# Kernel optimization log

Hardware: AMD Instinct MI355X
Metric: run time of the kernel (lower is better)

Reference implementation:

```python
import jax, jax.numpy as jnp
import numpy as np

C = 512
CQK = C // 8
B, H, W = 4, 128, 128

def setup_inputs() -> dict:
    key = jax.random.key(0)
    ks = jax.random.split(key, 8)
    x = jax.random.normal(ks[0], (B, C, H, W), dtype=jnp.float32)
    # 1x1 conv weights stored as [out, in]
    Wq = jax.random.normal(ks[1], (CQK, C), dtype=jnp.float32) * (1.0 / np.sqrt(C))
    bq = jax.random.normal(ks[2], (CQK,), dtype=jnp.float32) * 0.01
    Wk = jax.random.normal(ks[3], (CQK, C), dtype=jnp.float32) * (1.0 / np.sqrt(C))
    bk = jax.random.normal(ks[4], (CQK,), dtype=jnp.float32) * 0.01
    Wv = jax.random.normal(ks[5], (C, C), dtype=jnp.float32) * (1.0 / np.sqrt(C))
    bv = jax.random.normal(ks[6], (C,), dtype=jnp.float32) * 0.01
    gamma = jnp.zeros((1,), dtype=jnp.float32)
    return {"x": x, "Wq": Wq, "bq": bq, "Wk": Wk, "bk": bk, "Wv": Wv, "bv": bv, "gamma": gamma}

def _conv1x1(x, Wt, b):
    # x: [B,C,H,W], Wt: [O,C] -> [B,O,H,W]
    return jnp.einsum('bchw,oc->bohw', x, Wt) + b[None, :, None, None]

def reference(x, Wq, bq, Wk, bk, Wv, bv, gamma):
    q = _conv1x1(x, Wq, bq)   # [B,CQK,H,W]
    k = _conv1x1(x, Wk, bk)   # [B,CQK,H,W]
    v = _conv1x1(x, Wv, bv)   # [B,C,H,W]
    # axial attention along height, independently per (batch, width-column)
    energy = jnp.einsum('bchw,bcgw->bwhg', q, k)      # [B,W,H,H]
    attn = jax.nn.softmax(energy, axis=-1)
    out = jnp.einsum('bcgw,bwhg->bchw', v, attn)      # [B,C,H,W]
    return gamma * out + x
```

## Files before the change

### kernel.cpp

```cpp
#include <hip/hip_runtime.h>
#include <hip/hip_bf16.h>

typedef float f32x4  __attribute__((ext_vector_type(4)));
typedef int   v8i    __attribute__((ext_vector_type(8)));
typedef unsigned short u16;
typedef unsigned char  u8;

#define B_ 4
#define C_ 512
#define H_ 128
#define W_ 128
#define NO_ 640

__device__ __forceinline__ u16 f2bf(float f) {
    __hip_bfloat16 h = __float2bfloat16(f);
    union { __hip_bfloat16 h; u16 u; } cv; cv.h = h; return cv.u;
}
__device__ __forceinline__ unsigned f2fp8x2(float a, float b) {
    return (unsigned)__builtin_amdgcn_cvt_pk_fp8_f32(a, b, 0, false);
}
__device__ __forceinline__ u8 f2fp8(float f) {
    return (u8)(f2fp8x2(f, 0.f) & 0xFF);
}
__device__ __forceinline__ float fp82f(unsigned b) {
    const unsigned s = (b >> 7) & 1u, e = (b >> 3) & 15u, m = b & 7u;
    union { unsigned u; float f; } c;
    c.u = (s << 31) | ((e + 120u) << 23) | (m << 20);
    const float fs = (s ? -1.f : 1.f) * (float)m * 0.001953125f;
    return e ? c.f : fs;
}

__device__ __forceinline__ void gld16(const void* g, void* l) {
    __builtin_amdgcn_global_load_lds(
        (const __attribute__((address_space(1))) void*)g,
        (__attribute__((address_space(3))) void*)l, 16, 0, 0);
}

__global__ __launch_bounds__(256) void k_convw(const float* __restrict__ Wq, const float* __restrict__ bq,
                                               const float* __restrict__ Wk, const float* __restrict__ bk,
                                               const float* __restrict__ Wv, const float* __restrict__ bv,
                                               u8* __restrict__ Wcat, float* __restrict__ bcat) {
    const int idx = blockIdx.x * 256 + threadIdx.x;
    if (idx < NO_ * C_) {
        const int o = idx >> 9, c = idx & 511;
        float v;
        if (o < 64)       v = Wq[o * C_ + c];
        else if (o < 128) v = Wk[(o - 64) * C_ + c];
        else              v = Wv[(o - 128) * C_ + c];
        Wcat[idx] = f2fp8(v);
    }
    if (idx < NO_) {
        float v = (idx < 64) ? bq[idx] : ((idx < 128) ? bk[idx - 64] : bv[idx - 128]);
        bcat[idx] = v;
    }
}

__global__ __launch_bounds__(256) void k_transpose_x(const float* __restrict__ x, u8* __restrict__ xT) {
    __shared__ float tile[64][65];
    const int b  = blockIdx.x >> 7;
    const int h  = blockIdx.x & 127;
    const int c0 = (blockIdx.y >> 1) * 64;
    const int w0 = (blockIdx.y & 1) * 64;
    const int t = threadIdx.x, r = t >> 4, seg = t & 15;
    const float* xp = x + (size_t)b * C_ * H_ * W_ + (size_t)h * W_;
#pragma unroll
    for (int rr = 0; rr < 4; ++rr) {
        const int c = rr * 16 + r;
        float4 v = *(const float4*)(xp + (size_t)(c0 + c) * (H_ * W_) + w0 + seg * 4);
        tile[c][seg * 4 + 0] = v.x; tile[c][seg * 4 + 1] = v.y;
        tile[c][seg * 4 + 2] = v.z; tile[c][seg * 4 + 3] = v.w;
    }
    __syncthreads();
#pragma unroll
    for (int rr = 0; rr < 4; ++rr) {
        const int w = rr * 16 + r;
        const unsigned lo = f2fp8x2(tile[seg * 4 + 0][w], tile[seg * 4 + 1][w]);
        const unsigned hi = f2fp8x2(tile[seg * 4 + 2][w], tile[seg * 4 + 3][w]);
        *(unsigned*)(xT + ((size_t)((b * W_ + w0 + w) * H_ + h)) * C_ + c0 + seg * 4)
            = (lo & 0xFFFFu) | (hi << 16);
    }
}

__global__ __launch_bounds__(256, 2) void k_gemm(const u8* __restrict__ A, const u8* __restrict__ Wc,
                                                 const float* __restrict__ bias, u8* __restrict__ Call,
                                                 u8* __restrict__ vt) {
    __shared__ __align__(16) u8 smem[65536];
    const int t = threadIdx.x;
    const int lane = t & 63;
    const int wave = t >> 6;
    const int wr = wave >> 1;
    const int wc = wave & 1;
    const int lr = lane & 15;
    const int q4 = lane >> 4;

    const int bid = blockIdx.x;
    const int wg = (bid & 7) * 320 + (bid >> 3);
    const int panel = wg / 5;
    const int n = wg - panel * 5;
    const int r0 = panel * 128;
    const int n0 = n * 128;

    const int srow = t >> 3;
    const int slog = (t & 7) ^ (srow & 7);
    const u8* gA = A  + (size_t)(r0 + srow) * C_ + slog * 16;
    const u8* gB = Wc + (size_t)(n0 + srow) * C_ + slog * 16;

#define STAGE(KT) do {                                                   \
        u8* S_ = smem + ((KT) & 1) * 32768;                              \
        const int k0_ = (KT) * 128;                                      \
        gld16(gA + k0_,                    S_ + t * 16);                 \
        gld16(gA + (size_t)32 * C_ + k0_,  S_ + 4096  + t * 16);         \
        gld16(gA + (size_t)64 * C_ + k0_,  S_ + 8192  + t * 16);         \
        gld16(gA + (size_t)96 * C_ + k0_,  S_ + 12288 + t * 16);         \
        gld16(gB + k0_,                    S_ + 16384 + t * 16);         \
        gld16(gB + (size_t)32 * C_ + k0_,  S_ + 20480 + t * 16);         \
        gld16(gB + (size_t)64 * C_ + k0_,  S_ + 24576 + t * 16);         \
        gld16(gB + (size_t)96 * C_ + k0_,  S_ + 28672 + t * 16);         \
    } while (0)

    f32x4 acc[4][4] = {};
    STAGE(0);

#pragma unroll
    for (int T = 0; T < 4; ++T) {
        asm volatile("s_waitcnt vmcnt(0)" ::: "memory");
        __builtin_amdgcn_s_barrier();
        const u8* Ab = smem + (T & 1) * 32768;
        const u8* Bb = Ab + 16384;
        v8i fa[4], fb[4];
#pragma unroll
        for (int mi = 0; mi < 4; ++mi) {
            const int rr = wr * 64 + mi * 16 + lr;
            int4 lo = *(const int4*)&Ab[rr * 128 + (((2 * q4 + 0) ^ (rr & 7)) * 16)];
            int4 hi = *(const int4*)&Ab[rr * 128 + (((2 * q4 + 1) ^ (rr & 7)) * 16)];
            v8i f; f[0] = lo.x; f[1] = lo.y; f[2] = lo.z; f[3] = lo.w;
                   f[4] = hi.x; f[5] = hi.y; f[6] = hi.z; f[7] = hi.w;
            fa[mi] = f;
        }
#pragma unroll
        for (int ni = 0; ni < 4; ++ni) {
            const int rr = wc * 64 + ni * 16 + lr;
            int4 lo = *(const int4*)&Bb[rr * 128 + (((2 * q4 + 0) ^ (rr & 7)) * 16)];
            int4 hi = *(const int4*)&Bb[rr * 128 + (((2 * q4 + 1) ^ (rr & 7)) * 16)];
            v8i f; f[0] = lo.x; f[1] = lo.y; f[2] = lo.z; f[3] = lo.w;
                   f[4] = hi.x; f[5] = hi.y; f[6] = hi.z; f[7] = hi.w;
            fb[ni] = f;
        }
        if (T < 3) STAGE(T + 1);
        __builtin_amdgcn_s_setprio(1);
#pragma unroll
        for (int mi = 0; mi < 4; ++mi)
#pragma unroll
            for (int ni = 0; ni < 4; ++ni)
                acc[mi][ni] = __builtin_amdgcn_mfma_scale_f32_16x16x128_f8f6f4(
                    fa[mi], fb[ni], acc[mi][ni],
                    0, 0,
                    0, 0x7F7F7F7Fu,
                    0, 0x7F7F7F7Fu);
        __builtin_amdgcn_s_setprio(0);
    }
#undef STAGE
    __syncthreads();

    if (n == 0) {
#pragma unroll
        for (int ni = 0; ni < 4; ++ni) {
            const int o = wc * 64 + ni * 16 + lr;
            const float bz = bias[o];
#pragma unroll
            for (int mi = 0; mi < 4; ++mi)
#pragma unroll
                for (int j = 0; j < 4; ++j) {
                    const int rg = r0 + wr * 64 + mi * 16 + q4 * 4 + j;
                    Call[(size_t)rg * 128 + o] = f2fp8(acc[mi][ni][j] + bz);
                }
        }
    } else {
        u8* Tt = smem;
#pragma unroll
        for (int ni = 0; ni < 4; ++ni) {
            const int c_loc = wc * 64 + ni * 16 + lr;
            const float bz = bias[n0 + c_loc];
#pragma unroll
            for (int mi = 0; mi < 4; ++mi) {
                const int h = wr * 64 + mi * 16 + q4 * 4;
                unsigned p = f2fp8x2(acc[mi][ni][0] + bz, acc[mi][ni][1] + bz) & 0xFFFFu;
                p |= f2fp8x2(acc[mi][ni][2] + bz, acc[mi][ni][3] + bz) << 16;
                *(unsigned*)&Tt[c_loc * 144 + h] = p;
            }
        }
        __syncthreads();
        {
            const int c_loc = t >> 1;
            const int half  = t & 1;
            const int cg = (n - 1) * 128 + c_loc;
            u8* dst = vt + ((size_t)panel * 512 + cg) * 128 + half * 64;
            const u8* src = &Tt[c_loc * 144 + half * 64];
#pragma unroll
            for (int k = 0; k < 4; ++k)
                *(int4*)&dst[k * 16] = *(const int4*)&src[k * 16];
        }
    }
}

__global__ __launch_bounds__(256) void k_attn(const u8* __restrict__ Call, const u8* __restrict__ vt,
                                              u8* __restrict__ outws) {
    __shared__ __align__(16) float E[128][132];
    __shared__ float Rinv[128];
    const int bw = blockIdx.x;
    const int t = threadIdx.x;
    const int lane = t & 63;
    const int wr = t >> 7;
    const int wc = (t >> 6) & 1;
    const int lr = lane & 15, lk = (lane >> 4) * 8;
    const size_t rowbase = (size_t)bw * 128;

    f32x4 e[4][4] = {};
#pragma unroll
    for (int kk = 0; kk < 2; ++kk) {
        long fq[4], fk[4];
#pragma unroll
        for (int mi = 0; mi < 4; ++mi)
            fq[mi] = *(const long*)&Call[(rowbase + wr * 64 + mi * 16 + lr) * 128 + kk * 32 + lk];
#pragma unroll
        for (int ni = 0; ni < 4; ++ni)
            fk[ni] = *(const long*)&Call[(rowbase + wc * 64 + ni * 16 + lr) * 128 + 64 + kk * 32 + lk];
#pragma unroll
        for (int mi = 0; mi < 4; ++mi)
#pragma unroll
            for (int ni = 0; ni < 4; ++ni)
                e[mi][ni] = __builtin_amdgcn_mfma_f32_16x16x32_fp8_fp8(fq[mi], fk[ni], e[mi][ni], 0, 0, 0);
    }
#pragma unroll
    for (int mi = 0; mi < 4; ++mi)
#pragma unroll
        for (int ni = 0; ni < 4; ++ni)
#pragma unroll
            for (int j = 0; j < 4; ++j)
                E[wr * 64 + mi * 16 + (lane >> 4) * 4 + j][wc * 64 + ni * 16 + lr] = e[mi][ni][j];
    __syncthreads();

    {
        const int h = t >> 1, hf = (t & 1) * 64;
        float m = -1e30f;
        for (int i = 0; i < 64; ++i) m = fmaxf(m, E[h][hf + i]);
        m = fmaxf(m, __shfl_xor(m, 1));
        float s = 0.f;
        for (int i = 0; i < 64; ++i) {
            float p = __expf(E[h][hf + i] - m);
            E[h][hf + i] = p;
            s += p;
        }
        s += __shfl_xor(s, 1);
        if ((t & 1) == 0) Rinv[h] = 1.0f / s;
    }
    __syncthreads();

    float rv[4][4];
#pragma unroll
    for (int mi = 0; mi < 4; ++mi)
#pragma unroll
        for (int j = 0; j < 4; ++j)
            rv[mi][j] = Rinv[wr * 64 + mi * 16 + (lane >> 4) * 4 + j];

    long pa[4][4];
#pragma unroll
    for (int kk = 0; kk < 4; ++kk)
#pragma unroll
        for (int mi = 0; mi < 4; ++mi) {
            const float* ep = &E[wr * 64 + mi * 16 + lr][kk * 32 + lk];
            float4 v0 = *(const float4*)ep;
            float4 v1 = *(const float4*)(ep + 4);
            unsigned lo = (unsigned)__builtin_amdgcn_cvt_pk_fp8_f32(v0.x, v0.y, 0, false);
            lo = (unsigned)__builtin_amdgcn_cvt_pk_fp8_f32(v0.z, v0.w, (int)lo, true);
            unsigned hi = (unsigned)__builtin_amdgcn_cvt_pk_fp8_f32(v1.x, v1.y, 0, false);
            hi = (unsigned)__builtin_amdgcn_cvt_pk_fp8_f32(v1.z, v1.w, (int)hi, true);
            pa[kk][mi] = (long)lo | ((long)hi << 32);
        }

    for (int cc = 0; cc < 4; ++cc) {
        f32x4 acc[4][4] = {};
#pragma unroll
        for (int kk = 0; kk < 4; ++kk) {
            long fb[4];
#pragma unroll
            for (int ni = 0; ni < 4; ++ni)
                fb[ni] = *(const long*)&vt[((size_t)bw * 512 + cc * 128 + wc * 64 + ni * 16 + lr) * 128 + kk * 32 + lk];
#pragma unroll
            for (int mi = 0; mi < 4; ++mi)
#pragma unroll
                for (int ni = 0; ni < 4; ++ni)
                    acc[mi][ni] = __builtin_amdgcn_mfma_f32_16x16x32_fp8_fp8(pa[kk][mi], fb[ni], acc[mi][ni], 0, 0, 0);
        }
#pragma unroll
        for (int ni = 0; ni < 4; ++ni) {
            const int c = cc * 128 + wc * 64 + ni * 16 + lr;
#pragma unroll
            for (int mi = 0; mi < 4; ++mi)
#pragma unroll
                for (int j = 0; j < 4; ++j) {
                    const int hh = wr * 64 + mi * 16 + (lane >> 4) * 4 + j;
                    outws[(rowbase + hh) * 512 + c] = f2fp8(acc[mi][ni][j] * rv[mi][j]);
                }
        }
    }
}

__global__ __launch_bounds__(256) void k_merge(const u8* __restrict__ outws, const float* __restrict__ x,
                                               const float* __restrict__ gamma, float* __restrict__ out) {
    __shared__ float tile[64][65];
    const int b  = blockIdx.x >> 7;
    const int h  = blockIdx.x & 127;
    const int c0 = (blockIdx.y >> 1) * 64;
    const int w0 = (blockIdx.y & 1) * 64;
    const float g = gamma[0];
    const int t = threadIdx.x, r = t >> 4, seg = t & 15;
#pragma unroll
    for (int rr = 0; rr < 4; ++rr) {
        const int w = rr * 16 + r;
        unsigned v = *(const unsigned*)(outws + ((size_t)((b * W_ + w0 + w) * H_) + h) * C_ + c0 + seg * 4);
        tile[w][seg * 4 + 0] = fp82f(v & 0xFFu);
        tile[w][seg * 4 + 1] = fp82f((v >> 8) & 0xFFu);
        tile[w][seg * 4 + 2] = fp82f((v >> 16) & 0xFFu);
        tile[w][seg * 4 + 3] = fp82f(v >> 24);
    }
    __syncthreads();
#pragma unroll
    for (int rr = 0; rr < 4; ++rr) {
        const int c = rr * 16 + r;
        const size_t base = ((size_t)(b * C_ + c0 + c) * H_ + h) * W_ + w0 + seg * 4;
        float4 xv = *(const float4*)(x + base);
        float4 o;
        o.x = g * tile[seg * 4 + 0][c] + xv.x;
        o.y = g * tile[seg * 4 + 1][c] + xv.y;
        o.z = g * tile[seg * 4 + 2][c] + xv.z;
        o.w = g * tile[seg * 4 + 3][c] + xv.w;
        *(float4*)(out + base) = o;
    }
}

extern "C" void kernel_launch(void* const* d_in, const int* in_sizes, int n_in,
                              void* d_out, int out_size, void* d_ws, size_t ws_size,
                              hipStream_t stream) {
    const float* x     = (const float*)d_in[0];
    const float* Wq    = (const float*)d_in[1];
    const float* bq    = (const float*)d_in[2];
    const float* Wk    = (const float*)d_in[3];
    const float* bk    = (const float*)d_in[4];
    const float* Wv    = (const float*)d_in[5];
    const float* bv    = (const float*)d_in[6];
    const float* gamma = (const float*)d_in[7];

    char* ws = (char*)d_ws;
    u8*    Wcat  = (u8*)ws;
    float* bcat  = (float*)(ws + 655360);
    u8*    xT    = (u8*)(ws + (1u << 20));
    u8*    Call  = (u8*)(ws + (1u << 20) + 67108864);
    u8*    outws = (u8*)(ws + (1u << 20));
    u8*    vt    = (u8*)d_out;

    k_convw<<<dim3((NO_ * C_ + 255) / 256), 256, 0, stream>>>(Wq, bq, Wk, bk, Wv, bv, Wcat, bcat);
    k_transpose_x<<<dim3(B_ * H_, 16), 256, 0, stream>>>(x, xT);
    k_gemm<<<dim3(2560), 256, 0, stream>>>(xT, Wcat, bcat, Call, vt);
    k_attn<<<dim3(B_ * W_), 256, 0, stream>>>(Call, vt, outws);
    k_merge<<<dim3(B_ * H_, 16), 256, 0, stream>>>(outws, x, gamma, (float*)d_out);
}
```

Baseline: 154.5 us.

## Keep A panel resident in LDS and loop over all output column tiles per block

The GEMM now assigns one block per 128-row panel, loading the full 128x512 fp8 A panel into LDS once and streaming the five 128-column weight tiles through a double-buffered ring. Previously five separate blocks re-read the same A panel from global memory. The trade-off is fewer blocks (512 instead of 2560), about 114 KB of LDS per block so only one block fits per CU, and a longer serial chain of work per block with an extra barrier for each epilogue.

```diff
diff --git a/kernel.cpp b/kernel.cpp
--- a/kernel.cpp
+++ b/kernel.cpp
@@ -81,10 +81,13 @@
     }
 }
 
-__global__ __launch_bounds__(256, 2) void k_gemm(const u8* __restrict__ A, const u8* __restrict__ Wc,
-                                                 const float* __restrict__ bias, u8* __restrict__ Call,
-                                                 u8* __restrict__ vt) {
-    __shared__ __align__(16) u8 smem[65536];
+__global__ __launch_bounds__(256) void k_gemm(const u8* __restrict__ A, const u8* __restrict__ Wc,
+                                              const float* __restrict__ bias, u8* __restrict__ Call,
+                                              u8* __restrict__ vt) {
+    __shared__ __align__(16) u8 smem[116736];
+    u8* Asm   = smem;
+    u8* Bring = smem + 65536;
+    u8* Tt    = smem + 98304;
     const int t = threadIdx.x;
     const int lane = t & 63;
     const int wave = t >> 6;
@@ -93,50 +96,54 @@
     const int lr = lane & 15;
     const int q4 = lane >> 4;
 
-    const int bid = blockIdx.x;
-    const int wg = (bid & 7) * 320 + (bid >> 3);
-    const int panel = wg / 5;
-    const int n = wg - panel * 5;
+    const int panel = blockIdx.x;
     const int r0 = panel * 128;
-    const int n0 = n * 128;
-
-    const int srow = t >> 3;
-    const int slog = (t & 7) ^ (srow & 7);
-    const u8* gA = A  + (size_t)(r0 + srow) * C_ + slog * 16;
-    const u8* gB = Wc + (size_t)(n0 + srow) * C_ + slog * 16;
-
-#define STAGE(KT) do {                                                   \
-        u8* S_ = smem + ((KT) & 1) * 32768;                              \
-        const int k0_ = (KT) * 128;                                      \
-        gld16(gA + k0_,                    S_ + t * 16);                 \
-        gld16(gA + (size_t)32 * C_ + k0_,  S_ + 4096  + t * 16);         \
-        gld16(gA + (size_t)64 * C_ + k0_,  S_ + 8192  + t * 16);         \
-        gld16(gA + (size_t)96 * C_ + k0_,  S_ + 12288 + t * 16);         \
-        gld16(gB + k0_,                    S_ + 16384 + t * 16);         \
-        gld16(gB + (size_t)32 * C_ + k0_,  S_ + 20480 + t * 16);         \
-        gld16(gB + (size_t)64 * C_ + k0_,  S_ + 24576 + t * 16);         \
-        gld16(gB + (size_t)96 * C_ + k0_,  S_ + 28672 + t * 16);         \
+
+    const u8* gA = A + (size_t)(r0 + (t >> 5)) * C_ + (((t & 31) ^ ((t >> 5) & 7)) * 16);
+    const int brow = t >> 3;
+    const u8* gBbase = Wc + (size_t)brow * C_ + (((t & 7) ^ (brow & 7)) * 16);
+
+#define STAGE_B(NN, TT, SLOT) do {                                       \
+        u8* S_ = Bring + (SLOT) * 16384;                                 \
+        const u8* src_ = gBbase + (size_t)(NN) * 128 * C_ + (TT) * 128;  \
+        gld16(src_,          S_ + t * 16);                               \
+        gld16(src_ + 16384,  S_ + 4096  + t * 16);                       \
+        gld16(src_ + 32768,  S_ + 8192  + t * 16);                       \
+        gld16(src_ + 49152,  S_ + 12288 + t * 16);                       \
     } while (0)
 
-    f32x4 acc[4][4] = {};
-    STAGE(0);
-
-#pragma unroll
-    for (int T = 0; T < 4; ++T) {
+#pragma unroll
+    for (int r = 0; r < 16; ++r)
+        gld16(gA + (size_t)r * 4096, Asm + r * 4096 + t * 16);
+    STAGE_B(0, 0, 0);
+
+    f32x4 acc[4][4];
+
+#pragma unroll
+    for (int s = 0; s < 20; ++s) {
+        const int nn = s >> 2, TT = s & 3, slot = s & 1;
+        if (TT == 0) {
+#pragma unroll
+            for (int mi = 0; mi < 4; ++mi)
+#pragma unroll
+                for (int ni = 0; ni < 4; ++ni)
+                    acc[mi][ni] = (f32x4){0.f, 0.f, 0.f, 0.f};
+        }
         asm volatile("s_waitcnt vmcnt(0)" ::: "memory");
         __builtin_amdgcn_s_barrier();
-        const u8* Ab = smem + (T & 1) * 32768;
-        const u8* Bb = Ab + 16384;
+
         v8i fa[4], fb[4];
 #pragma unroll
         for (int mi = 0; mi < 4; ++mi) {
             const int rr = wr * 64 + mi * 16 + lr;
-            int4 lo = *(const int4*)&Ab[rr * 128 + (((2 * q4 + 0) ^ (rr & 7)) * 16)];
-            int4 hi = *(const int4*)&Ab[rr * 128 + (((2 * q4 + 1) ^ (rr & 7)) * 16)];
+            const int base = rr * 512 + TT * 128;
+            int4 lo = *(const int4*)&Asm[base + (((2 * q4 + 0) ^ (rr & 7)) * 16)];
+            int4 hi = *(const int4*)&Asm[base + (((2 * q4 + 1) ^ (rr & 7)) * 16)];
             v8i f; f[0] = lo.x; f[1] = lo.y; f[2] = lo.z; f[3] = lo.w;
                    f[4] = hi.x; f[5] = hi.y; f[6] = hi.z; f[7] = hi.w;
             fa[mi] = f;
         }
+        const u8* Bb = Bring + slot * 16384;
 #pragma unroll
         for (int ni = 0; ni < 4; ++ni) {
             const int rr = wc * 64 + ni * 16 + lr;
@@ -146,7 +153,8 @@
                    f[4] = hi.x; f[5] = hi.y; f[6] = hi.z; f[7] = hi.w;
             fb[ni] = f;
         }
-        if (T < 3) STAGE(T + 1);
+        if (s + 1 < 20) STAGE_B((s + 1) >> 2, (s + 1) & 3, (s + 1) & 1);
+
         __builtin_amdgcn_s_setprio(1);
 #pragma unroll
         for (int mi = 0; mi < 4; ++mi)
@@ -158,49 +166,51 @@
                     0, 0x7F7F7F7Fu,
                     0, 0x7F7F7F7Fu);
         __builtin_amdgcn_s_setprio(0);
-    }
-#undef STAGE
-    __syncthreads();
-
-    if (n == 0) {
-#pragma unroll
-        for (int ni = 0; ni < 4; ++ni) {
-            const int o = wc * 64 + ni * 16 + lr;
-            const float bz = bias[o];
-#pragma unroll
-            for (int mi = 0; mi < 4; ++mi)
-#pragma unroll
-                for (int j = 0; j < 4; ++j) {
-                    const int rg = r0 + wr * 64 + mi * 16 + q4 * 4 + j;
-                    Call[(size_t)rg * 128 + o] = f2fp8(acc[mi][ni][j] + bz);
+
+        if (TT == 3) {
+            if (nn == 0) {
+#pragma unroll
+                for (int ni = 0; ni < 4; ++ni) {
+                    const int o = wc * 64 + ni * 16 + lr;
+                    const float bz = bias[o];
+#pragma unroll
+                    for (int mi = 0; mi < 4; ++mi)
+#pragma unroll
+                        for (int j = 0; j < 4; ++j) {
+                            const int rg = r0 + wr * 64 + mi * 16 + q4 * 4 + j;
+                            Call[(size_t)rg * 128 + o] = f2fp8(acc[mi][ni][j] + bz);
+                        }
                 }
-        }
-    } else {
-        u8* Tt = smem;
-#pragma unroll
-        for (int ni = 0; ni < 4; ++ni) {
-            const int c_loc = wc * 64 + ni * 16 + lr;
-            const float bz = bias[n0 + c_loc];
-#pragma unroll
-            for (int mi = 0; mi < 4; ++mi) {
-                const int h = wr * 64 + mi * 16 + q4 * 4;
-                unsigned p = f2fp8x2(acc[mi][ni][0] + bz, acc[mi][ni][1] + bz) & 0xFFFFu;
-                p |= f2fp8x2(acc[mi][ni][2] + bz, acc[mi][ni][3] + bz) << 16;
-                *(unsigned*)&Tt[c_loc * 144 + h] = p;
+            } else {
+#pragma unroll
+                for (int ni = 0; ni < 4; ++ni) {
+                    const int c_loc = wc * 64 + ni * 16 + lr;
+                    const float bz = bias[nn * 128 + c_loc];
+#pragma unroll
+                    for (int mi = 0; mi < 4; ++mi) {
+                        const int h = wr * 64 + mi * 16 + q4 * 4;
+                        unsigned p = f2fp8x2(acc[mi][ni][0] + bz, acc[mi][ni][1] + bz) & 0xFFFFu;
+                        p |= f2fp8x2(acc[mi][ni][2] + bz, acc[mi][ni][3] + bz) << 16;
+                        *(unsigned*)&Tt[c_loc * 144 + h] = p;
+                    }
+                }
+                asm volatile("s_waitcnt lgkmcnt(0)" ::: "memory");
+                __builtin_amdgcn_sched_barrier(0);
+                __builtin_amdgcn_s_barrier();
+                {
+                    const int c_loc = t >> 1;
+                    const int half  = t & 1;
+                    const int cg = (nn - 1) * 128 + c_loc;
+                    u8* dst = vt + ((size_t)panel * 512 + cg) * 128 + half * 64;
+                    const u8* src = &Tt[c_loc * 144 + half * 64];
+#pragma unroll
+                    for (int k = 0; k < 4; ++k)
+                        *(int4*)&dst[k * 16] = *(const int4*)&src[k * 16];
+                }
             }
         }
-        __syncthreads();
-        {
-            const int c_loc = t >> 1;
-            const int half  = t & 1;
-            const int cg = (n - 1) * 128 + c_loc;
-            u8* dst = vt + ((size_t)panel * 512 + cg) * 128 + half * 64;
-            const u8* src = &Tt[c_loc * 144 + half * 64];
-#pragma unroll
-            for (int k = 0; k < 4; ++k)
-                *(int4*)&dst[k * 16] = *(const int4*)&src[k * 16];
-        }
-    }
+    }
+#undef STAGE_B
 }
 
 __global__ __launch_bounds__(256) void k_attn(const u8* __restrict__ Call, const u8* __restrict__ vt,
@@ -361,7 +371,7 @@
 
     k_convw<<<dim3((NO_ * C_ + 255) / 256), 256, 0, stream>>>(Wq, bq, Wk, bk, Wv, bv, Wcat, bcat);
     k_transpose_x<<<dim3(B_ * H_, 16), 256, 0, stream>>>(x, xT);
-    k_gemm<<<dim3(2560), 256, 0, stream>>>(xT, Wcat, bcat, Call, vt);
+    k_gemm<<<dim3(512), 256, 0, stream>>>(xT, Wcat, bcat, Call, vt);
     k_attn<<<dim3(B_ * W_), 256, 0, stream>>>(Call, vt, outws);
     k_merge<<<dim3(B_ * H_, 16), 256, 0, stream>>>(outws, x, gamma, (float*)d_out);
 }
```

New measurement: 173.3 us. 12.2% more time.
